# Kernel optimization log

Measured on AMD Instinct MI355X. Metric: run time of the kernel, lower is better.

Reference implementation:

```python
import math
import jax, jax.numpy as jnp
from jax import lax
import numpy as np

B, T, DIM = 2, 1024, 512
EXPAND, D_STATE, CONV_K, NUM_SCALES = 2, 16, 4, 3
D_INNER = EXPAND * DIM
DT_RANK = D_INNER // 16


def parallel_scan_log(log_coeffs, log_values):
    # h_t = a_t*h_{t-1} + b_t via Heinsen log-space scan
    a_star = jnp.cumsum(log_coeffs, axis=1)
    return jnp.exp(a_star + lax.cumlogsumexp(log_values - a_star, axis=1))


def selective_scan(x, dt, A, B_ssm, C_ssm, D_p):
    Bb, Tt, di = x.shape
    ds = A.shape[1]
    dt = jax.nn.softplus(dt)
    dA = jnp.exp(dt[..., None] * A[None, None])                    # (B,T,di,ds)
    dBx = dt[..., None] * B_ssm[:, :, None, :] * x[..., None]      # (B,T,di,ds)
    log_dA = jnp.log(jnp.maximum(dA, 1e-38)).reshape(Bb, Tt, di * ds)
    log_dBx = jnp.log(jnp.maximum(dBx, 1e-38)).reshape(Bb, Tt, di * ds)
    h = parallel_scan_log(log_dA, log_dBx).reshape(Bb, Tt, di, ds)
    return jnp.einsum('bts,btds->btd', C_ssm, h) + D_p * x


def ssm_core(x, conv_w, conv_b, xproj_w, dtproj_w, dtproj_b, A_log, D_p):
    di = x.shape[-1]
    # depthwise causal conv1d: left-pad K-1 (== torch pad K-1 both sides + truncate to T)
    xc = lax.conv_general_dilated(x.transpose(0, 2, 1), conv_w, (1,), [(CONV_K - 1, 0)],
                                  dimension_numbers=('NCH', 'OIH', 'NCH'),
                                  feature_group_count=di)
    xc = jax.nn.silu((xc + conv_b[None, :, None]).transpose(0, 2, 1))
    proj = xc @ xproj_w.T
    dt_raw = proj[..., :DT_RANK]
    B_ssm = proj[..., DT_RANK:DT_RANK + D_STATE]
    C_ssm = proj[..., DT_RANK + D_STATE:]
    dt = dt_raw @ dtproj_w.T + dtproj_b
    A = -jnp.exp(A_log)
    return selective_scan(xc, dt, A, B_ssm, C_ssm, D_p)


def downsample(x, stride):
    if stride == 1:
        return x
    Bb, Tt, Dd = x.shape
    Tt2 = Tt // stride * stride
    return x[:, :Tt2].reshape(Bb, Tt2 // stride, stride, Dd).mean(axis=2)


def upsample(x, T_target):
    Bb, T_src, Dd = x.shape
    if T_src == T_target:
        return x
    factor = math.ceil(T_target / T_src)
    x_up = jnp.repeat(x, factor, axis=1)[:, :T_target]
    if x_up.shape[1] < T_target:
        pad = jnp.broadcast_to(x_up[:, -1:], (Bb, T_target - x_up.shape[1], Dd))
        x_up = jnp.concatenate([x_up, pad], axis=1)
    return x_up


def forward(x, in_proj_w, conv_w, conv_b, xproj_w, dtproj_w, dtproj_b, A_log, D_p,
            scale_weights, cg_w1, cg_w2, out_proj_w, ln_gamma, ln_beta):
    Tt = x.shape[1]
    residual = x
    xz = x @ in_proj_w.T
    x_in, gate = xz[..., :D_INNER], xz[..., D_INNER:]
    outs = []
    for s in range(NUM_SCALES):
        x_s = downsample(x_in, 2 ** s)
        y_s = ssm_core(x_s, conv_w[s], conv_b[s], xproj_w[s], dtproj_w[s],
                       dtproj_b[s], A_log[s], D_p[s])
        outs.append(upsample(y_s, Tt))
    w = jax.nn.softmax(scale_weights)
    fused = sum(w[s] * outs[s] for s in range(NUM_SCALES))
    ctx = jnp.mean(jnp.stack(outs, axis=0), axis=0)
    cg = jax.nn.sigmoid(jax.nn.silu(ctx @ cg_w1.T) @ cg_w2.T)
    fused = fused * cg
    out = (fused * jax.nn.silu(gate)) @ out_proj_w.T
    y = out + residual
    mu = jnp.mean(y, axis=-1, keepdims=True)
    var = jnp.var(y, axis=-1, keepdims=True)
    return (y - mu) / jnp.sqrt(var + 1e-5) * ln_gamma + ln_beta


def setup_inputs():
    key = jax.random.key(0)
    ks = jax.random.split(key, 12)
    x = jax.random.normal(ks[0], (B, T, DIM), jnp.float32)
    in_proj_w = jax.random.normal(ks[1], (2 * D_INNER, DIM), jnp.float32) * (1.0 / math.sqrt(DIM))
    conv_w = jax.random.normal(ks[2], (NUM_SCALES, D_INNER, 1, CONV_K), jnp.float32) * 0.3
    conv_b = jax.random.normal(ks[3], (NUM_SCALES, D_INNER), jnp.float32) * 0.05
    xproj_w = jax.random.normal(ks[4], (NUM_SCALES, DT_RANK + 2 * D_STATE, D_INNER), jnp.float32) * 0.02
    dtproj_w = jax.random.normal(ks[5], (NUM_SCALES, D_INNER, DT_RANK), jnp.float32) * 0.05
    dtproj_b = jax.random.uniform(ks[6], (NUM_SCALES, D_INNER), jnp.float32,
                                  math.log(0.001), math.log(0.1))
    A_log = jnp.broadcast_to(jnp.log(jnp.arange(1, D_STATE + 1, dtype=jnp.float32)),
                             (NUM_SCALES, D_INNER, D_STATE))
    D_p = jnp.ones((NUM_SCALES, D_INNER), jnp.float32)
    scale_weights = jnp.ones((NUM_SCALES,), jnp.float32)
    cg_w1 = jax.random.normal(ks[7], (D_INNER // 2, D_INNER), jnp.float32) * (1.0 / math.sqrt(D_INNER))
    cg_w2 = jax.random.normal(ks[8], (D_INNER, D_INNER // 2), jnp.float32) * (1.0 / math.sqrt(D_INNER // 2))
    out_proj_w = jax.random.normal(ks[9], (DIM, D_INNER), jnp.float32) * (1.0 / math.sqrt(D_INNER))
    ln_gamma = jnp.ones((DIM,), jnp.float32)
    ln_beta = jnp.zeros((DIM,), jnp.float32)
    return {"x": x, "in_proj_w": in_proj_w, "conv_w": conv_w, "conv_b": conv_b,
            "xproj_w": xproj_w, "dtproj_w": dtproj_w, "dtproj_b": dtproj_b,
            "A_log": A_log, "D_p": D_p, "scale_weights": scale_weights,
            "cg_w1": cg_w1, "cg_w2": cg_w2, "out_proj_w": out_proj_w,
            "ln_gamma": ln_gamma, "ln_beta": ln_beta}


def reference(x, in_proj_w, conv_w, conv_b, xproj_w, dtproj_w, dtproj_b, A_log, D_p,
              scale_weights, cg_w1, cg_w2, out_proj_w, ln_gamma, ln_beta):
    return forward(x, in_proj_w, conv_w, conv_b, xproj_w, dtproj_w, dtproj_b, A_log,
                   D_p, scale_weights, cg_w1, cg_w2, out_proj_w, ln_gamma, ln_beta)
```

## Files before the change

kernel.cpp:

```cpp
#include <hip/hip_runtime.h>
#include <hip/hip_bf16.h>

#define BATCH   2
#define SEQ     1024
#define DIMSZ   512
#define DINNER  1024
#define DTRANK  64
#define DSTATE  16
#define CHUNK   32

typedef __hip_bfloat16 bf16;
typedef __attribute__((ext_vector_type(8))) short s8v;
typedef __attribute__((ext_vector_type(4))) float f4v;

constexpr size_t OXI   = 0;
constexpr size_t OIPI  = 2097152;
constexpr size_t OXWI  = 4194304;
constexpr size_t ODTI  = 4784128;
constexpr size_t OC1I  = 5177344;
constexpr size_t OC2I  = 6225920;
constexpr size_t OOPI  = 7274496;
constexpr size_t OPJI  = 8323072;
constexpr size_t OFGI  = 10878976;

__device__ __forceinline__ float sigmoidf_(float x) { return 1.f / (1.f + __expf(-x)); }
__device__ __forceinline__ float siluf_(float x) { return x * sigmoidf_(x); }
__device__ __forceinline__ void split2(float v, bf16& hi, bf16& lo) {
    hi = __float2bfloat16(v);
    lo = __float2bfloat16(v - __bfloat162float(hi));
}
__device__ __forceinline__ void split_store4i(const float4 v, bf16* __restrict__ p) {
    union { bf16 b[8]; uint4 q; } U;
    split2(v.x, U.b[0], U.b[4]); split2(v.y, U.b[1], U.b[5]);
    split2(v.z, U.b[2], U.b[6]); split2(v.w, U.b[3], U.b[7]);
    *reinterpret_cast<uint4*>(p) = U.q;
}
__device__ __forceinline__ void split_store4(const float4 v,
                                             bf16* __restrict__ ph,
                                             bf16* __restrict__ pl) {
    union { bf16 b[4]; uint2 u; } H, L;
    split2(v.x, H.b[0], L.b[0]); split2(v.y, H.b[1], L.b[1]);
    split2(v.z, H.b[2], L.b[2]); split2(v.w, H.b[3], L.b[3]);
    *reinterpret_cast<uint2*>(ph) = H.u;
    *reinterpret_cast<uint2*>(pl) = L.u;
}

__global__ void split_inputs_kernel(
    const float* __restrict__ x,   const float* __restrict__ ipw,
    const float* __restrict__ xw,  const float* __restrict__ dtw,
    const float* __restrict__ c1,  const float* __restrict__ c2,
    const float* __restrict__ opw, bf16* __restrict__ bws)
{
    int blk = blockIdx.x;
    const float* src; size_t off;
    if (blk < 1024)      { src = x;   off = OXI;  }
    else if (blk < 2048) { src = ipw; off = OIPI; blk -= 1024; }
    else if (blk < 2336) { src = xw;  off = OXWI; blk -= 2048; }
    else if (blk < 2528) { src = dtw; off = ODTI; blk -= 2336; }
    else if (blk < 3040) { src = c1;  off = OC1I; blk -= 2528; }
    else if (blk < 3552) { src = c2;  off = OC2I; blk -= 3040; }
    else                 { src = opw; off = OOPI; blk -= 3552; }
    int i = blk * 1024 + threadIdx.x * 4;
    float4 v = *reinterpret_cast<const float4*>(src + i);
    split_store4i(v, bws + off + (size_t)i * 2);
}

template <int ACT, bool ADD_RES, bool DT_MODE, int AMODE, bool GATE3, bool OUT_SPLIT>
__global__ __launch_bounds__(256) void mgemm_kernel(
    const bf16* __restrict__ Ai, int lda, int K, int ldb,
    const bf16* __restrict__ Bi,
    const float* __restrict__ bias,
    const float* __restrict__ res,
    const float* __restrict__ gxz,
    const float* __restrict__ yy0,
    const float* __restrict__ yy1,
    const float* __restrict__ yy2,
    const float* __restrict__ sa0,
    const float* __restrict__ sa1,
    const float* __restrict__ swp,
    float* __restrict__ C, bf16* __restrict__ Ci, int N)
{
    __shared__ bf16 Ah[64][72], Al[64][72], Bh[64][72], Bl[64][72];

    const int m0 = blockIdx.x * 64;
    const int n0 = blockIdx.y * 64;
    const int kz = blockIdx.z;
    const int koff = kz * K;
    const size_t coff = (size_t)kz * (size_t)(gridDim.x * 64) * N;
    const int tid = threadIdx.x;
    const int wave = tid >> 6;
    const int lane = tid & 63;
    const int wm = (wave >> 1) * 32;
    const int wn = (wave & 1) * 32;
    const int m16 = lane & 15;
    const int q   = lane >> 4;

    int scale = 0;
    if (DT_MODE) scale = (m0 < 2048) ? 0 : ((m0 < 3072) ? 1 : 2);
    const bf16* Bip = DT_MODE ? (Bi + (size_t)scale * 1024 * ldb * 2) : Bi;
    const float* bias_p = (ACT == 3) ? (DT_MODE ? bias + (size_t)scale * N : bias) : nullptr;

    f4v acc[2][2];
#pragma unroll
    for (int i = 0; i < 2; i++)
#pragma unroll
        for (int j = 0; j < 2; j++)
#pragma unroll
            for (int r = 0; r < 4; r++) acc[i][j][r] = 0.f;

    const int cch = tid & 15;
    const int c4  = cch * 4;
    const int r0  = tid >> 4;

    const float* a0p[4]; const float* a1p[4]; const float* a2p[4];
    const float* s0p[4]; const float* s1p[4];
    const bf16*  aip[4];
#pragma unroll
    for (int p = 0; p < 4; p++) {
        int m = m0 + r0 + p * 16;
        if (AMODE == 1) {
            int b = m >> 10, t = m & 1023;
            a0p[p] = yy0 + koff + (size_t)m * 1024 + c4;
            a1p[p] = yy1 + koff + (size_t)((b << 9) + (t >> 1)) * 1024 + c4;
            a2p[p] = yy2 + koff + (size_t)((b << 8) + (t >> 2)) * 1024 + c4;
        } else if (AMODE == 2) {
            s0p[p] = sa0 + koff + (size_t)m * lda + c4;
            s1p[p] = sa1 + koff + (size_t)m * lda + c4;
        } else {
            aip[p] = Ai + ((size_t)m * lda + koff + c4) * 2;
        }
    }
    const bf16* Bi_b = Bip + ((size_t)(n0 + r0) * ldb + koff + c4) * 2;

    const int nkt = K >> 6;
    float4 raf[4]; uint2 rah[4], ral[4], rbh[4], rbl[4];
#pragma unroll
    for (int p = 0; p < 4; p++) {
        if (AMODE == 1) {
            float4 u = *reinterpret_cast<const float4*>(a0p[p]);
            float4 v = *reinterpret_cast<const float4*>(a1p[p]);
            float4 w = *reinterpret_cast<const float4*>(a2p[p]);
            raf[p] = make_float4((u.x + v.x + w.x) * (1.f / 3.f), (u.y + v.y + w.y) * (1.f / 3.f),
                                 (u.z + v.z + w.z) * (1.f / 3.f), (u.w + v.w + w.w) * (1.f / 3.f));
        } else if (AMODE == 2) {
            float4 u = *reinterpret_cast<const float4*>(s0p[p]);
            float4 v = *reinterpret_cast<const float4*>(s1p[p]);
            raf[p] = make_float4(siluf_(u.x + v.x), siluf_(u.y + v.y),
                                 siluf_(u.z + v.z), siluf_(u.w + v.w));
        } else {
            uint4 ua = *reinterpret_cast<const uint4*>(aip[p]);
            rah[p] = make_uint2(ua.x, ua.y); ral[p] = make_uint2(ua.z, ua.w);
        }
        uint4 ub = *reinterpret_cast<const uint4*>(Bi_b + (size_t)(p * 16) * ldb * 2);
        rbh[p] = make_uint2(ub.x, ub.y); rbl[p] = make_uint2(ub.z, ub.w);
    }

    for (int kt = 0; kt < nkt; kt++) {
        if (kt) __syncthreads();
#pragma unroll
        for (int p = 0; p < 4; p++) {
            int r = r0 + p * 16;
            if (AMODE != 0) {
                split_store4(raf[p], &Ah[r][c4], &Al[r][c4]);
            } else {
                *reinterpret_cast<uint2*>(&Ah[r][c4]) = rah[p];
                *reinterpret_cast<uint2*>(&Al[r][c4]) = ral[p];
            }
            *reinterpret_cast<uint2*>(&Bh[r][c4]) = rbh[p];
            *reinterpret_cast<uint2*>(&Bl[r][c4]) = rbl[p];
        }
        __syncthreads();
        if (kt + 1 < nkt) {
            int off = (kt + 1) * 64;
#pragma unroll
            for (int p = 0; p < 4; p++) {
                if (AMODE == 1) {
                    float4 u = *reinterpret_cast<const float4*>(a0p[p] + off);
                    float4 v = *reinterpret_cast<const float4*>(a1p[p] + off);
                    float4 w = *reinterpret_cast<const float4*>(a2p[p] + off);
                    raf[p] = make_float4((u.x + v.x + w.x) * (1.f / 3.f), (u.y + v.y + w.y) * (1.f / 3.f),
                                         (u.z + v.z + w.z) * (1.f / 3.f), (u.w + v.w + w.w) * (1.f / 3.f));
                } else if (AMODE == 2) {
                    float4 u = *reinterpret_cast<const float4*>(s0p[p] + off);
                    float4 v = *reinterpret_cast<const float4*>(s1p[p] + off);
                    raf[p] = make_float4(siluf_(u.x + v.x), siluf_(u.y + v.y),
                                         siluf_(u.z + v.z), siluf_(u.w + v.w));
                } else {
                    uint4 ua = *reinterpret_cast<const uint4*>(aip[p] + (size_t)off * 2);
                    rah[p] = make_uint2(ua.x, ua.y); ral[p] = make_uint2(ua.z, ua.w);
                }
                uint4 ub = *reinterpret_cast<const uint4*>(Bi_b + ((size_t)(p * 16) * ldb + off) * 2);
                rbh[p] = make_uint2(ub.x, ub.y); rbl[p] = make_uint2(ub.z, ub.w);
            }
        }
#pragma unroll
        for (int kk = 0; kk < 2; kk++) {
            const int col = kk * 32 + q * 8;
            s8v ah[2], al[2], bh[2], bl[2];
#pragma unroll
            for (int i = 0; i < 2; i++) {
                int ar = wm + i * 16 + m16;
                ah[i] = *reinterpret_cast<const s8v*>(&Ah[ar][col]);
                al[i] = *reinterpret_cast<const s8v*>(&Al[ar][col]);
                int br = wn + i * 16 + m16;
                bh[i] = *reinterpret_cast<const s8v*>(&Bh[br][col]);
                bl[i] = *reinterpret_cast<const s8v*>(&Bl[br][col]);
            }
#pragma unroll
            for (int i = 0; i < 2; i++)
#pragma unroll
                for (int j = 0; j < 2; j++) {
                    acc[i][j] = __builtin_amdgcn_mfma_f32_16x16x32_bf16(ah[i], bh[j], acc[i][j], 0, 0, 0);
                    acc[i][j] = __builtin_amdgcn_mfma_f32_16x16x32_bf16(al[i], bh[j], acc[i][j], 0, 0, 0);
                    acc[i][j] = __builtin_amdgcn_mfma_f32_16x16x32_bf16(ah[i], bl[j], acc[i][j], 0, 0, 0);
                }
        }
    }

    float e0 = 0.f, e1 = 0.f, e2 = 0.f, inv = 0.f;
    if (GATE3) {
        float s0 = swp[0], s1 = swp[1], s2 = swp[2];
        float mx = fmaxf(s0, fmaxf(s1, s2));
        e0 = __expf(s0 - mx); e1 = __expf(s1 - mx); e2 = __expf(s2 - mx);
        inv = 1.f / (e0 + e1 + e2);
    }

#pragma unroll
    for (int i = 0; i < 2; i++) {
#pragma unroll
        for (int j = 0; j < 2; j++) {
#pragma unroll
            for (int r = 0; r < 4; r++) {
                int gm = m0 + wm + i * 16 + q * 4 + r;
                int gn = n0 + wn + j * 16 + m16;
                float v = acc[i][j][r];
                if (ACT == 3) { v += bias_p[gn]; v = (v > 20.f) ? v : __logf(1.f + __expf(v)); }
                else if (ACT == 1) v = siluf_(v);
                else if (ACT == 2) v = sigmoidf_(v);
                if (GATE3) {
                    int b = gm >> 10, t = gm & 1023;
                    float f = (e0 * yy0[(size_t)gm * 1024 + gn]
                             + e1 * yy1[(size_t)((b << 9) + (t >> 1)) * 1024 + gn]
                             + e2 * yy2[(size_t)((b << 8) + (t >> 2)) * 1024 + gn]) * inv;
                    v = f * v * siluf_(gxz[(size_t)gm * 2048 + 1024 + gn]);
                } else if (ADD_RES) {
                    if (kz == 0) v += res[(size_t)gm * N + gn];
                }
                if (OUT_SPLIT) {
                    bf16 hh, ll; split2(v, hh, ll);
                    size_t gb = ((size_t)gm * N + (gn & ~3)) * 2 + (gn & 3);
                    Ci[gb] = hh;
                    Ci[gb + 4] = ll;
                } else {
                    C[coff + (size_t)gm * N + gn] = v;
                }
            }
        }
    }
}

__global__ __launch_bounds__(256) void xproj_mfma_kernel(
    const float* __restrict__ A,
    const bf16* __restrict__ xwi,
    float* __restrict__ pjp)
{
    __shared__ bf16 Ah[64][72], Al[64][72], Bh[64][72], Bl[64][72];

    const int m0 = blockIdx.x * 64;
    const int n0 = blockIdx.y * 64;
    const int kz = blockIdx.z;
    const int koff = kz * 512;
    const int tid = threadIdx.x;
    const int wave = tid >> 6;
    const int lane = tid & 63;
    const int wm = (wave >> 1) * 32;
    const int wn = (wave & 1) * 32;
    const int m16 = lane & 15;
    const int q   = lane >> 4;

    const int scale = (m0 < 2048) ? 0 : ((m0 < 3072) ? 1 : 2);
    const bf16* Bip = xwi + (size_t)scale * 96 * 1024 * 2;

    f4v acc[2][2];
#pragma unroll
    for (int i = 0; i < 2; i++)
#pragma unroll
        for (int j = 0; j < 2; j++)
#pragma unroll
            for (int r = 0; r < 4; r++) acc[i][j][r] = 0.f;

    const int cch = tid & 15;
    const int c4  = cch * 4;
    const int r0  = tid >> 4;

    const float* Abase = A + (size_t)(m0 + r0) * 1024 + koff + c4;
    const bf16* Bi_b = Bip + ((size_t)(n0 + r0) * 1024 + koff + c4) * 2;
    bool bok[4];
#pragma unroll
    for (int p = 0; p < 4; p++) bok[p] = (n0 + r0 + p * 16) < 96;

    const int nkt = 8;
    float4 ra[4]; uint2 rbh[4], rbl[4];
#pragma unroll
    for (int p = 0; p < 4; p++) {
        ra[p] = *reinterpret_cast<const float4*>(Abase + (size_t)(p * 16) * 1024);
        if (bok[p]) {
            uint4 ub = *reinterpret_cast<const uint4*>(Bi_b + (size_t)(p * 16) * 1024 * 2);
            rbh[p] = make_uint2(ub.x, ub.y); rbl[p] = make_uint2(ub.z, ub.w);
        } else { rbh[p] = make_uint2(0u, 0u); rbl[p] = make_uint2(0u, 0u); }
    }

    for (int kt = 0; kt < nkt; kt++) {
        if (kt) __syncthreads();
#pragma unroll
        for (int p = 0; p < 4; p++) {
            int r = r0 + p * 16;
            split_store4(ra[p], &Ah[r][c4], &Al[r][c4]);
            *reinterpret_cast<uint2*>(&Bh[r][c4]) = rbh[p];
            *reinterpret_cast<uint2*>(&Bl[r][c4]) = rbl[p];
        }
        __syncthreads();
        if (kt + 1 < nkt) {
            int off = (kt + 1) * 64;
#pragma unroll
            for (int p = 0; p < 4; p++) {
                ra[p] = *reinterpret_cast<const float4*>(Abase + off + (size_t)(p * 16) * 1024);
                if (bok[p]) {
                    uint4 ub = *reinterpret_cast<const uint4*>(Bi_b + ((size_t)(p * 16) * 1024 + off) * 2);
                    rbh[p] = make_uint2(ub.x, ub.y); rbl[p] = make_uint2(ub.z, ub.w);
                }
            }
        }
#pragma unroll
        for (int kk = 0; kk < 2; kk++) {
            const int col = kk * 32 + q * 8;
            s8v ah[2], al[2], bh[2], bl[2];
#pragma unroll
            for (int i = 0; i < 2; i++) {
                int ar = wm + i * 16 + m16;
                ah[i] = *reinterpret_cast<const s8v*>(&Ah[ar][col]);
                al[i] = *reinterpret_cast<const s8v*>(&Al[ar][col]);
                int br = wn + i * 16 + m16;
                bh[i] = *reinterpret_cast<const s8v*>(&Bh[br][col]);
                bl[i] = *reinterpret_cast<const s8v*>(&Bl[br][col]);
            }
#pragma unroll
            for (int i = 0; i < 2; i++)
#pragma unroll
                for (int j = 0; j < 2; j++) {
                    acc[i][j] = __builtin_amdgcn_mfma_f32_16x16x32_bf16(ah[i], bh[j], acc[i][j], 0, 0, 0);
                    acc[i][j] = __builtin_amdgcn_mfma_f32_16x16x32_bf16(al[i], bh[j], acc[i][j], 0, 0, 0);
                    acc[i][j] = __builtin_amdgcn_mfma_f32_16x16x32_bf16(ah[i], bl[j], acc[i][j], 0, 0, 0);
                }
        }
    }

    float* out = pjp + (size_t)kz * 344064;
#pragma unroll
    for (int i = 0; i < 2; i++) {
#pragma unroll
        for (int j = 0; j < 2; j++) {
            int gn = n0 + wn + j * 16 + m16;
            if (gn >= 96) continue;
#pragma unroll
            for (int r = 0; r < 4; r++) {
                int gm = m0 + wm + i * 16 + q * 4 + r;
                out[(size_t)gm * 96 + gn] = acc[i][j][r];
            }
        }
    }
}

__global__ void combine_pj_kernel(const float* __restrict__ pjp,
                                  float* __restrict__ pj,
                                  bf16* __restrict__ pjdti)
{
    int g = blockIdx.x * 256 + threadIdx.x;
    if (g >= 86016) return;
    int gm = g / 24;
    int gc = (g % 24) * 4;
    size_t o = (size_t)gm * 96 + gc;
    float4 a = *reinterpret_cast<const float4*>(pjp + o);
    float4 b = *reinterpret_cast<const float4*>(pjp + 344064 + o);
    float4 s = make_float4(a.x + b.x, a.y + b.y, a.z + b.z, a.w + b.w);
    *reinterpret_cast<float4*>(pj + o) = s;
    if (gc < 64) split_store4i(s, pjdti + ((size_t)gm * 64 + gc) * 2);
}

__global__ void conv_fused_kernel(const float* __restrict__ xz,
                                  const float* __restrict__ cw,
                                  const float* __restrict__ cb,
                                  float* __restrict__ xc)
{
    int idx = blockIdx.x * blockDim.x + threadIdx.x;
    if (idx >= 3670016) return;
    int s, rel;
    if (idx < 2097152)      { s = 0; rel = idx; }
    else if (idx < 3145728) { s = 1; rel = idx - 2097152; }
    else                    { s = 2; rel = idx - 3145728; }
    int c = rel & 1023;
    int row = rel >> 10;
    int Ts = 1024 >> s;
    int b = row / Ts;
    int t = row - b * Ts;
    const float* base = xz + (size_t)(b * 1024) * 2048 + c;

    float acc = cb[s * 1024 + c];
#pragma unroll
    for (int k = 0; k < 4; k++) {
        int tau = t - 3 + k;
        if (tau < 0) continue;
        float xv;
        if (s == 0) {
            xv = base[(size_t)tau * 2048];
        } else if (s == 1) {
            xv = 0.5f * (base[(size_t)(2 * tau) * 2048] + base[(size_t)(2 * tau + 1) * 2048]);
        } else {
            xv = 0.25f * (base[(size_t)(4 * tau) * 2048] + base[(size_t)(4 * tau + 1) * 2048]
                        + base[(size_t)(4 * tau + 2) * 2048] + base[(size_t)(4 * tau + 3) * 2048]);
        }
        acc = fmaf(cw[(s * 1024 + c) * 4 + k], xv, acc);
    }
    xc[idx] = siluf_(acc);
}

__device__ __forceinline__ void scan_decode(int blk, int& s, int& nchunk, int& Ts,
                                            int& dquad, int& chunk, int& b, size_t& soff)
{
    int local;
    if (blk < 256)      { s = 0; local = blk;       soff = 0; }
    else if (blk < 384) { s = 1; local = blk - 256; soff = 1048576; }
    else                { s = 2; local = blk - 384; soff = 1572864; }
    nchunk = 32 >> s;
    Ts = 1024 >> s;
    dquad = local & 3;
    chunk = (local >> 2) & (nchunk - 1);
    b = local >> (7 - s);
}

__global__ __launch_bounds__(256) void scan_pass1(
    const float* __restrict__ dt0, const float* __restrict__ xc0, const float* __restrict__ pj0,
    const float* __restrict__ dt1, const float* __restrict__ xc1, const float* __restrict__ pj1,
    const float* __restrict__ dt2, const float* __restrict__ xc2, const float* __restrict__ pj2,
    const float* __restrict__ A_log,
    float* __restrict__ prodA_buf, float* __restrict__ h_buf)
{
    const int jhalf = (blockIdx.x >= 448) ? 1 : 0;
    const int jo = jhalf * 8;
    int s, nchunk, Ts, dquad, chunk, b; size_t soff;
    scan_decode(blockIdx.x - jhalf * 448, s, nchunk, Ts, dquad, chunk, b, soff);
    const float* dt = (s == 0) ? dt0 : (s == 1) ? dt1 : dt2;
    const float* xc = (s == 0) ? xc0 : (s == 1) ? xc1 : xc2;
    const float* pj = (s == 0) ? pj0 : (s == 1) ? pj1 : pj2;

    const int d = dquad * 256 + threadIdx.x;
    const size_t rowbase = (size_t)b * Ts;
    const int t0 = chunk * CHUNK;

    float Acoef[8], h[8], p[8];
#pragma unroll
    for (int j = 0; j < 8; j++) {
        Acoef[j] = -__expf(A_log[((size_t)(s * DINNER + d)) * 16 + jo + j]);
        h[j] = 0.f; p[j] = 1.f;
    }

    __shared__ float bcB[CHUNK][8];
    if (threadIdx.x < CHUNK * 8) {
        int i = threadIdx.x >> 3, jj = threadIdx.x & 7;
        bcB[i][jj] = pj[(rowbase + t0 + i) * 96 + 64 + jo + jj];
    }
    __syncthreads();

    for (int i = 0; i < CHUNK; i++) {
        size_t t = rowbase + t0 + i;
        float dtv = dt[t * DINNER + d];
        float xv  = xc[t * DINNER + d];
#pragma unroll
        for (int j = 0; j < 8; j++) {
            float dA  = fmaxf(__expf(dtv * Acoef[j]), 1e-38f);
            float dbx = fmaxf(dtv * bcB[i][j] * xv, 1e-38f);
            h[j] = fmaf(dA, h[j], dbx);
            p[j] *= dA;
        }
    }

    size_t base = soff + (size_t)((b * nchunk + chunk) * 16 + jo) * 1024 + d;
#pragma unroll
    for (int j = 0; j < 8; j++) {
        prodA_buf[base + (size_t)j * 1024] = p[j];
        h_buf[base + (size_t)j * 1024] = h[j];
    }
}

__global__ __launch_bounds__(256) void scan_prefix_kernel(
    const float* __restrict__ prodA_buf, float* __restrict__ h_buf)
{
    int blk = blockIdx.x;
    int s; size_t soff;
    if (blk < 128)      { s = 0; soff = 0; }
    else if (blk < 256) { s = 1; soff = 1048576; blk -= 128; }
    else                { s = 2; soff = 1572864; blk -= 256; }
    const int nchunk = 32 >> s;
    const int b  = blk >> 6;
    const int j  = (blk >> 2) & 15;
    const int dq = blk & 3;
    const int d  = dq * 256 + threadIdx.x;

    float H = 0.f;
    for (int c = 0; c < nchunk; c++) {
        size_t idx = soff + (size_t)((b * nchunk + c) * 16 + j) * 1024 + d;
        float p = prodA_buf[idx];
        float h = h_buf[idx];
        h_buf[idx] = H;
        H = fmaf(p, H, h);
    }
}

__global__ __launch_bounds__(256) void scan_pass2(
    const float* __restrict__ dt0, const float* __restrict__ xc0,
    const float* __restrict__ pj0,
    const float* __restrict__ dt1, const float* __restrict__ xc1,
    const float* __restrict__ pj1,
    const float* __restrict__ dt2, const float* __restrict__ xc2,
    const float* __restrict__ pj2,
    float* __restrict__ y0, float* __restrict__ y1, float* __restrict__ y2,
    const float* __restrict__ A_log, const float* __restrict__ D_p,
    const float* __restrict__ carry)
{
    int s, nchunk, Ts, dquad, chunk, b; size_t soff;
    scan_decode(blockIdx.x, s, nchunk, Ts, dquad, chunk, b, soff);
    const float* dt = (s == 0) ? dt0 : (s == 1) ? dt1 : dt2;
    const float* xc = (s == 0) ? xc0 : (s == 1) ? xc1 : xc2;
    const float* pj = (s == 0) ? pj0 : (s == 1) ? pj1 : pj2;
    float* y = (s == 0) ? y0 : (s == 1) ? y1 : y2;

    const int d = dquad * 256 + threadIdx.x;
    const size_t rowbase = (size_t)b * Ts;
    const int t0 = chunk * CHUNK;

    float Acoef[16], h[16];
    const size_t cb = soff + (size_t)((b * nchunk + chunk) * 16) * 1024 + d;
#pragma unroll
    for (int j = 0; j < 16; j++) {
        Acoef[j] = -__expf(A_log[((size_t)(s * DINNER + d)) * 16 + j]);
        h[j] = carry[cb + (size_t)j * 1024];
    }
    const float Dp = D_p[s * DINNER + d];

    __shared__ float bc[CHUNK][32];
    for (int u = threadIdx.x; u < CHUNK * 32; u += 256) {
        int i = u >> 5, jj = u & 31;
        bc[i][jj] = pj[(rowbase + t0 + i) * 96 + 64 + jj];
    }
    __syncthreads();

    for (int i = 0; i < CHUNK; i++) {
        size_t t = rowbase + t0 + i;
        float dtv = dt[t * DINNER + d];
        float xv  = xc[t * DINNER + d];
        float accy = 0.f;
#pragma unroll
        for (int j = 0; j < 16; j++) {
            float dA  = fmaxf(__expf(dtv * Acoef[j]), 1e-38f);
            float dbx = fmaxf(dtv * bc[i][j] * xv, 1e-38f);
            h[j] = fmaf(dA, h[j], dbx);
            accy = fmaf(bc[i][16 + j], h[j], accy);
        }
        y[t * DINNER + d] = accy + Dp * xv;
    }
}

__global__ __launch_bounds__(256) void ln_kernel(
    const float* __restrict__ ya, const float* __restrict__ yb,
    const float* __restrict__ gamma,
    const float* __restrict__ beta, float* __restrict__ out)
{
    int token = blockIdx.x;
    int tid = threadIdx.x;
    size_t o = (size_t)token * DIMSZ;
    float v0 = ya[o + tid] + yb[o + tid];
    float v1 = ya[o + tid + 256] + yb[o + tid + 256];
    __shared__ float s1[256], s2[256];
    s1[tid] = v0 + v1;
    s2[tid] = v0 * v0 + v1 * v1;
    __syncthreads();
    for (int off = 128; off > 0; off >>= 1) {
        if (tid < off) { s1[tid] += s1[tid + off]; s2[tid] += s2[tid + off]; }
        __syncthreads();
    }
    float mu = s1[0] * (1.f / 512.f);
    float var = s2[0] * (1.f / 512.f) - mu * mu;
    float rstd = rsqrtf(var + 1e-5f);
    float* orow = out + o;
    orow[tid]       = (v0 - mu) * rstd * gamma[tid]       + beta[tid];
    orow[tid + 256] = (v1 - mu) * rstd * gamma[tid + 256] + beta[tid + 256];
}

extern "C" void kernel_launch(void* const* d_in, const int* in_sizes, int n_in,
                              void* d_out, int out_size, void* d_ws, size_t ws_size,
                              hipStream_t stream)
{
    const float* x         = (const float*)d_in[0];
    const float* in_proj_w = (const float*)d_in[1];
    const float* conv_w    = (const float*)d_in[2];
    const float* conv_b    = (const float*)d_in[3];
    const float* xproj_w   = (const float*)d_in[4];
    const float* dtproj_w  = (const float*)d_in[5];
    const float* dtproj_b  = (const float*)d_in[6];
    const float* A_log     = (const float*)d_in[7];
    const float* D_p       = (const float*)d_in[8];
    const float* scale_w   = (const float*)d_in[9];
    const float* cg_w1     = (const float*)d_in[10];
    const float* cg_w2     = (const float*)d_in[11];
    const float* out_pw    = (const float*)d_in[12];
    const float* ln_gamma  = (const float*)d_in[13];
    const float* ln_beta   = (const float*)d_in[14];
    float* out = (float*)d_out;

    float* ws = (float*)d_ws;
    float* xz    = ws;
    float* xc0   = xz    + 4194304;
    float* xc1   = xc0   + 2097152;
    float* xc2   = xc1   + 1048576;
    float* pj0   = xc2   + 524288;
    float* pj1   = pj0   + 196608;
    float* pj2   = pj1   + 98304;
    float* dt0   = pj2   + 49152;
    float* dt1   = dt0   + 2097152;
    float* dt2   = dt1   + 1048576;
    float* y0    = dt2   + 524288;
    float* y1    = y0    + 2097152;
    float* y2    = y1    + 1048576;
    float* hole  = y2    + 524288;
    float* prodA = hole  + 3670016;
    float* hbuf  = prodA + 1835008;

    float* pjp   = hole;
    float* h1p   = hole + 688128;
    float* outp  = prodA;

    bf16* bws = (bf16*)(ws + 23887872);
    const bf16 *xi   = bws + OXI;
    const bf16 *ipwi = bws + OIPI;
    const bf16 *xwi  = bws + OXWI;
    const bf16 *dtwi = bws + ODTI;
    const bf16 *c1i  = bws + OC1I;
    const bf16 *c2i  = bws + OC2I;
    const bf16 *opwi = bws + OOPI;
    bf16 *pjdti = bws + OPJI;
    bf16 *fgi   = bws + OFGI;

    split_inputs_kernel<<<4064, 256, 0, stream>>>(
        x, in_proj_w, xproj_w, dtproj_w, cg_w1, cg_w2, out_pw, bws);

    mgemm_kernel<0, false, false, 0, false, false><<<dim3(32, 32), 256, 0, stream>>>(
        xi, 512, 512, 512, ipwi, nullptr, nullptr, nullptr,
        nullptr, nullptr, nullptr, nullptr, nullptr, nullptr, xz, nullptr, 2048);

    conv_fused_kernel<<<14336, 256, 0, stream>>>(xz, conv_w, conv_b, xc0);

    xproj_mfma_kernel<<<dim3(56, 2, 2), 256, 0, stream>>>(xc0, xwi, pjp);

    combine_pj_kernel<<<336, 256, 0, stream>>>(pjp, pj0, pjdti);

    mgemm_kernel<3, false, true, 0, false, false><<<dim3(56, 16), 256, 0, stream>>>(
        pjdti, 64, 64, 64, dtwi, dtproj_b, nullptr, nullptr,
        nullptr, nullptr, nullptr, nullptr, nullptr, nullptr, dt0, nullptr, 1024);

    scan_pass1<<<896, 256, 0, stream>>>(dt0, xc0, pj0, dt1, xc1, pj1,
                                        dt2, xc2, pj2, A_log, prodA, hbuf);
    scan_prefix_kernel<<<384, 256, 0, stream>>>(prodA, hbuf);
    scan_pass2<<<448, 256, 0, stream>>>(dt0, xc0, pj0, dt1, xc1, pj1,
                                        dt2, xc2, pj2,
                                        y0, y1, y2, A_log, D_p, hbuf);

    mgemm_kernel<0, false, false, 1, false, false><<<dim3(32, 8, 2), 256, 0, stream>>>(
        nullptr, 1024, 512, 1024, c1i, nullptr, nullptr, nullptr,
        y0, y1, y2, nullptr, nullptr, nullptr, h1p, nullptr, 512);

    mgemm_kernel<2, false, false, 2, true, true><<<dim3(32, 16), 256, 0, stream>>>(
        nullptr, 512, 512, 512, c2i, nullptr, nullptr, xz,
        y0, y1, y2, h1p, h1p + 1048576, scale_w, nullptr, fgi, 1024);

    mgemm_kernel<0, true, false, 0, false, false><<<dim3(32, 8, 2), 256, 0, stream>>>(
        fgi, 1024, 512, 1024, opwi, nullptr, x, nullptr,
        nullptr, nullptr, nullptr, nullptr, nullptr, nullptr, outp, nullptr, 512);

    ln_kernel<<<BATCH * SEQ, 256, 0, stream>>>(outp, outp + 1048576,
                                               ln_gamma, ln_beta, out);
}
```

Baseline: 270.0 us.

## Split xproj K four ways, drop combine kernel, precompute scale-fused context once

The x-projection GEMM now splits K into four partial sums instead of two. The separate combine kernel is removed, and consumers (the dt GEMM through a new 4-input A mode, and both scan passes) sum the partials on load. A new yfuse kernel computes the scale-mean context in split bf16 and the softmax-weighted fused output once. This replaces recomputing them inside the cg GEMM A-load loop and epilogue, which read three y buffers per tile. The trade is an extra launch plus extra memory writes and reads for the ctx and fused buffers, and redundant partial-sum reads in the scan kernels.

```diff
diff --git a/kernel.cpp b/kernel.cpp
--- a/kernel.cpp
+++ b/kernel.cpp
@@ -20,8 +20,10 @@
 constexpr size_t OC1I  = 5177344;
 constexpr size_t OC2I  = 6225920;
 constexpr size_t OOPI  = 7274496;
-constexpr size_t OPJI  = 8323072;
 constexpr size_t OFGI  = 10878976;
+constexpr size_t OCTXI = 15073280;
+
+constexpr size_t PJP_STRIDE = 344064;
 
 __device__ __forceinline__ float sigmoidf_(float x) { return 1.f / (1.f + __expf(-x)); }
 __device__ __forceinline__ float siluf_(float x) { return x * sigmoidf_(x); }
@@ -65,19 +67,18 @@
     split_store4i(v, bws + off + (size_t)i * 2);
 }
 
-template <int ACT, bool ADD_RES, bool DT_MODE, int AMODE, bool GATE3, bool OUT_SPLIT>
+template <int ACT, bool ADD_RES, bool DT_MODE, int AMODE, bool GATEF, bool OUT_SPLIT>
 __global__ __launch_bounds__(256) void mgemm_kernel(
     const bf16* __restrict__ Ai, int lda, int K, int ldb,
     const bf16* __restrict__ Bi,
     const float* __restrict__ bias,
     const float* __restrict__ res,
     const float* __restrict__ gxz,
-    const float* __restrict__ yy0,
-    const float* __restrict__ yy1,
-    const float* __restrict__ yy2,
+    const float* __restrict__ fw,
     const float* __restrict__ sa0,
     const float* __restrict__ sa1,
-    const float* __restrict__ swp,
+    const float* __restrict__ sa2,
+    const float* __restrict__ sa3,
     float* __restrict__ C, bf16* __restrict__ Ci, int N)
 {
     __shared__ bf16 Ah[64][72], Al[64][72], Bh[64][72], Bl[64][72];
@@ -112,20 +113,19 @@
     const int c4  = cch * 4;
     const int r0  = tid >> 4;
 
-    const float* a0p[4]; const float* a1p[4]; const float* a2p[4];
-    const float* s0p[4]; const float* s1p[4];
+    const float* s0p[4]; const float* s1p[4]; const float* s2p[4]; const float* s3p[4];
     const bf16*  aip[4];
 #pragma unroll
     for (int p = 0; p < 4; p++) {
         int m = m0 + r0 + p * 16;
-        if (AMODE == 1) {
-            int b = m >> 10, t = m & 1023;
-            a0p[p] = yy0 + koff + (size_t)m * 1024 + c4;
-            a1p[p] = yy1 + koff + (size_t)((b << 9) + (t >> 1)) * 1024 + c4;
-            a2p[p] = yy2 + koff + (size_t)((b << 8) + (t >> 2)) * 1024 + c4;
-        } else if (AMODE == 2) {
+        if (AMODE == 2) {
             s0p[p] = sa0 + koff + (size_t)m * lda + c4;
             s1p[p] = sa1 + koff + (size_t)m * lda + c4;
+        } else if (AMODE == 3) {
+            s0p[p] = sa0 + koff + (size_t)m * lda + c4;
+            s1p[p] = sa1 + koff + (size_t)m * lda + c4;
+            s2p[p] = sa2 + koff + (size_t)m * lda + c4;
+            s3p[p] = sa3 + koff + (size_t)m * lda + c4;
         } else {
             aip[p] = Ai + ((size_t)m * lda + koff + c4) * 2;
         }
@@ -136,17 +136,18 @@
     float4 raf[4]; uint2 rah[4], ral[4], rbh[4], rbl[4];
 #pragma unroll
     for (int p = 0; p < 4; p++) {
-        if (AMODE == 1) {
-            float4 u = *reinterpret_cast<const float4*>(a0p[p]);
-            float4 v = *reinterpret_cast<const float4*>(a1p[p]);
-            float4 w = *reinterpret_cast<const float4*>(a2p[p]);
-            raf[p] = make_float4((u.x + v.x + w.x) * (1.f / 3.f), (u.y + v.y + w.y) * (1.f / 3.f),
-                                 (u.z + v.z + w.z) * (1.f / 3.f), (u.w + v.w + w.w) * (1.f / 3.f));
-        } else if (AMODE == 2) {
+        if (AMODE == 2) {
             float4 u = *reinterpret_cast<const float4*>(s0p[p]);
             float4 v = *reinterpret_cast<const float4*>(s1p[p]);
             raf[p] = make_float4(siluf_(u.x + v.x), siluf_(u.y + v.y),
                                  siluf_(u.z + v.z), siluf_(u.w + v.w));
+        } else if (AMODE == 3) {
+            float4 u = *reinterpret_cast<const float4*>(s0p[p]);
+            float4 v = *reinterpret_cast<const float4*>(s1p[p]);
+            float4 w = *reinterpret_cast<const float4*>(s2p[p]);
+            float4 z = *reinterpret_cast<const float4*>(s3p[p]);
+            raf[p] = make_float4(u.x + v.x + w.x + z.x, u.y + v.y + w.y + z.y,
+                                 u.z + v.z + w.z + z.z, u.w + v.w + w.w + z.w);
         } else {
             uint4 ua = *reinterpret_cast<const uint4*>(aip[p]);
             rah[p] = make_uint2(ua.x, ua.y); ral[p] = make_uint2(ua.z, ua.w);
@@ -174,17 +175,18 @@
             int off = (kt + 1) * 64;
 #pragma unroll
             for (int p = 0; p < 4; p++) {
-                if (AMODE == 1) {
-                    float4 u = *reinterpret_cast<const float4*>(a0p[p] + off);
-                    float4 v = *reinterpret_cast<const float4*>(a1p[p] + off);
-                    float4 w = *reinterpret_cast<const float4*>(a2p[p] + off);
-                    raf[p] = make_float4((u.x + v.x + w.x) * (1.f / 3.f), (u.y + v.y + w.y) * (1.f / 3.f),
-                                         (u.z + v.z + w.z) * (1.f / 3.f), (u.w + v.w + w.w) * (1.f / 3.f));
-                } else if (AMODE == 2) {
+                if (AMODE == 2) {
                     float4 u = *reinterpret_cast<const float4*>(s0p[p] + off);
                     float4 v = *reinterpret_cast<const float4*>(s1p[p] + off);
                     raf[p] = make_float4(siluf_(u.x + v.x), siluf_(u.y + v.y),
                                          siluf_(u.z + v.z), siluf_(u.w + v.w));
+                } else if (AMODE == 3) {
+                    float4 u = *reinterpret_cast<const float4*>(s0p[p] + off);
+                    float4 v = *reinterpret_cast<const float4*>(s1p[p] + off);
+                    float4 w = *reinterpret_cast<const float4*>(s2p[p] + off);
+                    float4 z = *reinterpret_cast<const float4*>(s3p[p] + off);
+                    raf[p] = make_float4(u.x + v.x + w.x + z.x, u.y + v.y + w.y + z.y,
+                                         u.z + v.z + w.z + z.z, u.w + v.w + w.w + z.w);
                 } else {
                     uint4 ua = *reinterpret_cast<const uint4*>(aip[p] + (size_t)off * 2);
                     rah[p] = make_uint2(ua.x, ua.y); ral[p] = make_uint2(ua.z, ua.w);
@@ -217,14 +219,6 @@
         }
     }
 
-    float e0 = 0.f, e1 = 0.f, e2 = 0.f, inv = 0.f;
-    if (GATE3) {
-        float s0 = swp[0], s1 = swp[1], s2 = swp[2];
-        float mx = fmaxf(s0, fmaxf(s1, s2));
-        e0 = __expf(s0 - mx); e1 = __expf(s1 - mx); e2 = __expf(s2 - mx);
-        inv = 1.f / (e0 + e1 + e2);
-    }
-
 #pragma unroll
     for (int i = 0; i < 2; i++) {
 #pragma unroll
@@ -237,11 +231,8 @@
                 if (ACT == 3) { v += bias_p[gn]; v = (v > 20.f) ? v : __logf(1.f + __expf(v)); }
                 else if (ACT == 1) v = siluf_(v);
                 else if (ACT == 2) v = sigmoidf_(v);
-                if (GATE3) {
-                    int b = gm >> 10, t = gm & 1023;
-                    float f = (e0 * yy0[(size_t)gm * 1024 + gn]
-                             + e1 * yy1[(size_t)((b << 9) + (t >> 1)) * 1024 + gn]
-                             + e2 * yy2[(size_t)((b << 8) + (t >> 2)) * 1024 + gn]) * inv;
+                if (GATEF) {
+                    float f = fw[(size_t)gm * N + gn];
                     v = f * v * siluf_(gxz[(size_t)gm * 2048 + 1024 + gn]);
                 } else if (ADD_RES) {
                     if (kz == 0) v += res[(size_t)gm * N + gn];
@@ -269,7 +260,7 @@
     const int m0 = blockIdx.x * 64;
     const int n0 = blockIdx.y * 64;
     const int kz = blockIdx.z;
-    const int koff = kz * 512;
+    const int koff = kz * 256;
     const int tid = threadIdx.x;
     const int wave = tid >> 6;
     const int lane = tid & 63;
@@ -299,7 +290,7 @@
 #pragma unroll
     for (int p = 0; p < 4; p++) bok[p] = (n0 + r0 + p * 16) < 96;
 
-    const int nkt = 8;
+    const int nkt = 4;
     float4 ra[4]; uint2 rbh[4], rbl[4];
 #pragma unroll
     for (int p = 0; p < 4; p++) {
@@ -355,7 +346,7 @@
         }
     }
 
-    float* out = pjp + (size_t)kz * 344064;
+    float* out = pjp + (size_t)kz * PJP_STRIDE;
 #pragma unroll
     for (int i = 0; i < 2; i++) {
 #pragma unroll
@@ -369,22 +360,6 @@
             }
         }
     }
-}
-
-__global__ void combine_pj_kernel(const float* __restrict__ pjp,
-                                  float* __restrict__ pj,
-                                  bf16* __restrict__ pjdti)
-{
-    int g = blockIdx.x * 256 + threadIdx.x;
-    if (g >= 86016) return;
-    int gm = g / 24;
-    int gc = (g % 24) * 4;
-    size_t o = (size_t)gm * 96 + gc;
-    float4 a = *reinterpret_cast<const float4*>(pjp + o);
-    float4 b = *reinterpret_cast<const float4*>(pjp + 344064 + o);
-    float4 s = make_float4(a.x + b.x, a.y + b.y, a.z + b.z, a.w + b.w);
-    *reinterpret_cast<float4*>(pj + o) = s;
-    if (gc < 64) split_store4i(s, pjdti + ((size_t)gm * 64 + gc) * 2);
 }
 
 __global__ void conv_fused_kernel(const float* __restrict__ xz,
@@ -438,10 +413,16 @@
     b = local >> (7 - s);
 }
 
+__device__ __forceinline__ float pjp_sum(const float* __restrict__ pjp, size_t o)
+{
+    return pjp[o] + pjp[PJP_STRIDE + o] + pjp[2 * PJP_STRIDE + o] + pjp[3 * PJP_STRIDE + o];
+}
+
 __global__ __launch_bounds__(256) void scan_pass1(
-    const float* __restrict__ dt0, const float* __restrict__ xc0, const float* __restrict__ pj0,
-    const float* __restrict__ dt1, const float* __restrict__ xc1, const float* __restrict__ pj1,
-    const float* __restrict__ dt2, const float* __restrict__ xc2, const float* __restrict__ pj2,
+    const float* __restrict__ dt0, const float* __restrict__ xc0,
+    const float* __restrict__ dt1, const float* __restrict__ xc1,
+    const float* __restrict__ dt2, const float* __restrict__ xc2,
+    const float* __restrict__ pjp,
     const float* __restrict__ A_log,
     float* __restrict__ prodA_buf, float* __restrict__ h_buf)
 {
@@ -451,7 +432,7 @@
     scan_decode(blockIdx.x - jhalf * 448, s, nchunk, Ts, dquad, chunk, b, soff);
     const float* dt = (s == 0) ? dt0 : (s == 1) ? dt1 : dt2;
     const float* xc = (s == 0) ? xc0 : (s == 1) ? xc1 : xc2;
-    const float* pj = (s == 0) ? pj0 : (s == 1) ? pj1 : pj2;
+    const int srow = ((s == 0) ? 0 : (s == 1) ? 2048 : 3072) + b * Ts;
 
     const int d = dquad * 256 + threadIdx.x;
     const size_t rowbase = (size_t)b * Ts;
@@ -467,7 +448,8 @@
     __shared__ float bcB[CHUNK][8];
     if (threadIdx.x < CHUNK * 8) {
         int i = threadIdx.x >> 3, jj = threadIdx.x & 7;
-        bcB[i][jj] = pj[(rowbase + t0 + i) * 96 + 64 + jo + jj];
+        size_t o = (size_t)(srow + t0 + i) * 96 + 64 + jo + jj;
+        bcB[i][jj] = pjp_sum(pjp, o);
     }
     __syncthreads();
 
@@ -518,11 +500,9 @@
 
 __global__ __launch_bounds__(256) void scan_pass2(
     const float* __restrict__ dt0, const float* __restrict__ xc0,
-    const float* __restrict__ pj0,
     const float* __restrict__ dt1, const float* __restrict__ xc1,
-    const float* __restrict__ pj1,
     const float* __restrict__ dt2, const float* __restrict__ xc2,
-    const float* __restrict__ pj2,
+    const float* __restrict__ pjp,
     float* __restrict__ y0, float* __restrict__ y1, float* __restrict__ y2,
     const float* __restrict__ A_log, const float* __restrict__ D_p,
     const float* __restrict__ carry)
@@ -531,8 +511,8 @@
     scan_decode(blockIdx.x, s, nchunk, Ts, dquad, chunk, b, soff);
     const float* dt = (s == 0) ? dt0 : (s == 1) ? dt1 : dt2;
     const float* xc = (s == 0) ? xc0 : (s == 1) ? xc1 : xc2;
-    const float* pj = (s == 0) ? pj0 : (s == 1) ? pj1 : pj2;
     float* y = (s == 0) ? y0 : (s == 1) ? y1 : y2;
+    const int srow = ((s == 0) ? 0 : (s == 1) ? 2048 : 3072) + b * Ts;
 
     const int d = dquad * 256 + threadIdx.x;
     const size_t rowbase = (size_t)b * Ts;
@@ -550,7 +530,8 @@
     __shared__ float bc[CHUNK][32];
     for (int u = threadIdx.x; u < CHUNK * 32; u += 256) {
         int i = u >> 5, jj = u & 31;
-        bc[i][jj] = pj[(rowbase + t0 + i) * 96 + 64 + jj];
+        size_t o = (size_t)(srow + t0 + i) * 96 + 64 + jj;
+        bc[i][jj] = pjp_sum(pjp, o);
     }
     __syncthreads();
 
@@ -568,6 +549,35 @@
         }
         y[t * DINNER + d] = accy + Dp * xv;
     }
+}
+
+__global__ void yfuse_kernel(const float* __restrict__ y0,
+                             const float* __restrict__ y1,
+                             const float* __restrict__ y2,
+                             const float* __restrict__ swp,
+                             bf16* __restrict__ ctxi,
+                             float* __restrict__ fw)
+{
+    int g = blockIdx.x * 256 + threadIdx.x;
+    int m = g >> 8;
+    int k = (g & 255) << 2;
+    int b = m >> 10, t = m & 1023;
+    float4 u = *reinterpret_cast<const float4*>(y0 + (size_t)m * 1024 + k);
+    float4 v = *reinterpret_cast<const float4*>(y1 + (size_t)((b << 9) + (t >> 1)) * 1024 + k);
+    float4 w = *reinterpret_cast<const float4*>(y2 + (size_t)((b << 8) + (t >> 2)) * 1024 + k);
+    float4 c = make_float4((u.x + v.x + w.x) * (1.f / 3.f), (u.y + v.y + w.y) * (1.f / 3.f),
+                           (u.z + v.z + w.z) * (1.f / 3.f), (u.w + v.w + w.w) * (1.f / 3.f));
+    split_store4i(c, ctxi + ((size_t)m * 1024 + k) * 2);
+
+    float s0 = swp[0], s1 = swp[1], s2 = swp[2];
+    float mx = fmaxf(s0, fmaxf(s1, s2));
+    float e0 = __expf(s0 - mx), e1 = __expf(s1 - mx), e2 = __expf(s2 - mx);
+    float inv = 1.f / (e0 + e1 + e2);
+    float4 f = make_float4((e0 * u.x + e1 * v.x + e2 * w.x) * inv,
+                           (e0 * u.y + e1 * v.y + e2 * w.y) * inv,
+                           (e0 * u.z + e1 * v.z + e2 * w.z) * inv,
+                           (e0 * u.w + e1 * v.w + e2 * w.w) * inv);
+    *reinterpret_cast<float4*>(fw + (size_t)m * 1024 + k) = f;
 }
 
 __global__ __launch_bounds__(256) void ln_kernel(
@@ -622,10 +632,8 @@
     float* xc0   = xz    + 4194304;
     float* xc1   = xc0   + 2097152;
     float* xc2   = xc1   + 1048576;
-    float* pj0   = xc2   + 524288;
-    float* pj1   = pj0   + 196608;
-    float* pj2   = pj1   + 98304;
-    float* dt0   = pj2   + 49152;
+    float* pjfree= xc2   + 524288;
+    float* dt0   = pjfree+ 344064;
     float* dt1   = dt0   + 2097152;
     float* dt2   = dt1   + 1048576;
     float* y0    = dt2   + 524288;
@@ -636,8 +644,9 @@
     float* hbuf  = prodA + 1835008;
 
     float* pjp   = hole;
-    float* h1p   = hole + 688128;
-    float* outp  = prodA;
+    float* h1p   = hole + 1376256;
+    float* fusedw = prodA;
+    float* outp   = xc0;
 
     bf16* bws = (bf16*)(ws + 23887872);
     const bf16 *xi   = bws + OXI;
@@ -647,44 +656,44 @@
     const bf16 *c1i  = bws + OC1I;
     const bf16 *c2i  = bws + OC2I;
     const bf16 *opwi = bws + OOPI;
-    bf16 *pjdti = bws + OPJI;
     bf16 *fgi   = bws + OFGI;
+    bf16 *ctxi  = bws + OCTXI;
 
     split_inputs_kernel<<<4064, 256, 0, stream>>>(
         x, in_proj_w, xproj_w, dtproj_w, cg_w1, cg_w2, out_pw, bws);
 
     mgemm_kernel<0, false, false, 0, false, false><<<dim3(32, 32), 256, 0, stream>>>(
-        xi, 512, 512, 512, ipwi, nullptr, nullptr, nullptr,
-        nullptr, nullptr, nullptr, nullptr, nullptr, nullptr, xz, nullptr, 2048);
+        xi, 512, 512, 512, ipwi, nullptr, nullptr, nullptr, nullptr,
+        nullptr, nullptr, nullptr, nullptr, xz, nullptr, 2048);
 
     conv_fused_kernel<<<14336, 256, 0, stream>>>(xz, conv_w, conv_b, xc0);
 
-    xproj_mfma_kernel<<<dim3(56, 2, 2), 256, 0, stream>>>(xc0, xwi, pjp);
-
-    combine_pj_kernel<<<336, 256, 0, stream>>>(pjp, pj0, pjdti);
-
-    mgemm_kernel<3, false, true, 0, false, false><<<dim3(56, 16), 256, 0, stream>>>(
-        pjdti, 64, 64, 64, dtwi, dtproj_b, nullptr, nullptr,
-        nullptr, nullptr, nullptr, nullptr, nullptr, nullptr, dt0, nullptr, 1024);
-
-    scan_pass1<<<896, 256, 0, stream>>>(dt0, xc0, pj0, dt1, xc1, pj1,
-                                        dt2, xc2, pj2, A_log, prodA, hbuf);
+    xproj_mfma_kernel<<<dim3(56, 2, 4), 256, 0, stream>>>(xc0, xwi, pjp);
+
+    mgemm_kernel<3, false, true, 3, false, false><<<dim3(56, 16), 256, 0, stream>>>(
+        nullptr, 96, 64, 64, dtwi, dtproj_b, nullptr, nullptr, nullptr,
+        pjp, pjp + PJP_STRIDE, pjp + 2 * PJP_STRIDE, pjp + 3 * PJP_STRIDE,
+        dt0, nullptr, 1024);
+
+    scan_pass1<<<896, 256, 0, stream>>>(dt0, xc0, dt1, xc1, dt2, xc2,
+                                        pjp, A_log, prodA, hbuf);
     scan_prefix_kernel<<<384, 256, 0, stream>>>(prodA, hbuf);
-    scan_pass2<<<448, 256, 0, stream>>>(dt0, xc0, pj0, dt1, xc1, pj1,
-                                        dt2, xc2, pj2,
-                                        y0, y1, y2, A_log, D_p, hbuf);
-
-    mgemm_kernel<0, false, false, 1, false, false><<<dim3(32, 8, 2), 256, 0, stream>>>(
-        nullptr, 1024, 512, 1024, c1i, nullptr, nullptr, nullptr,
-        y0, y1, y2, nullptr, nullptr, nullptr, h1p, nullptr, 512);
+    scan_pass2<<<448, 256, 0, stream>>>(dt0, xc0, dt1, xc1, dt2, xc2,
+                                        pjp, y0, y1, y2, A_log, D_p, hbuf);
+
+    yfuse_kernel<<<2048, 256, 0, stream>>>(y0, y1, y2, scale_w, ctxi, fusedw);
+
+    mgemm_kernel<0, false, false, 0, false, false><<<dim3(32, 8, 2), 256, 0, stream>>>(
+        ctxi, 1024, 512, 1024, c1i, nullptr, nullptr, nullptr, nullptr,
+        nullptr, nullptr, nullptr, nullptr, h1p, nullptr, 512);
 
     mgemm_kernel<2, false, false, 2, true, true><<<dim3(32, 16), 256, 0, stream>>>(
-        nullptr, 512, 512, 512, c2i, nullptr, nullptr, xz,
-        y0, y1, y2, h1p, h1p + 1048576, scale_w, nullptr, fgi, 1024);
+        nullptr, 512, 512, 512, c2i, nullptr, nullptr, xz, fusedw,
+        h1p, h1p + 1048576, nullptr, nullptr, nullptr, fgi, 1024);
 
     mgemm_kernel<0, true, false, 0, false, false><<<dim3(32, 8, 2), 256, 0, stream>>>(
-        fgi, 1024, 512, 1024, opwi, nullptr, x, nullptr,
-        nullptr, nullptr, nullptr, nullptr, nullptr, nullptr, outp, nullptr, 512);
+        fgi, 1024, 512, 1024, opwi, nullptr, x, nullptr, nullptr,
+        nullptr, nullptr, nullptr, nullptr, outp, nullptr, 512);
 
     ln_kernel<<<BATCH * SEQ, 256, 0, stream>>>(outp, outp + 1048576,
                                                ln_gamma, ln_beta, out);
```

Result: slower. 277.8 us (+2.9%).
